# Kernel tuning notes

Hardware: AMD Instinct MI355X
Metric: run time of the kernel (lower is better)

The kernel has to match this reference:

```python
import jax, jax.numpy as jnp
import numpy as np

K, D, B, T = 512, 256, 32, 4096

def setup_inputs() -> dict:
    key = jax.random.key(0)
    k1, k2 = jax.random.split(key)
    z_e_x = jax.random.normal(k1, (B, D, T), dtype=jnp.float32)
    # nn.Embedding weight init uniform(-1/K, 1/K)
    emb_weight = jax.random.uniform(k2, (K, D), dtype=jnp.float32, minval=-1.0 / K, maxval=1.0 / K)
    return {"z_e_x": z_e_x, "emb_weight": emb_weight}

def reference(z_e_x, emb_weight):
    # forward(): permute [B,D,T] -> [B,T,D], nearest-codebook indices
    z = jnp.transpose(z_e_x, (0, 2, 1))  # [B, T, D]
    # squared L2 distances: ||z||^2 - 2 z.W^T + ||W||^2  -> [B, T, K]
    z_sq = jnp.sum(z * z, axis=-1, keepdims=True)           # [B, T, 1]
    w_sq = jnp.sum(emb_weight * emb_weight, axis=-1)        # [K]
    cross = jnp.einsum('btd,kd->btk', z, emb_weight)        # [B, T, K]
    dists = z_sq - 2.0 * cross + w_sq[None, None, :]
    latents = jnp.argmin(dists, axis=-1)                    # [B, T] int
    return latents
```

## Files before the change

kernel.cpp:

```cpp
#include <hip/hip_runtime.h>
#include <math.h>

#define NK 512
#define DD 256
#define NB 32
#define NT 4096

typedef __attribute__((ext_vector_type(8))) _Float16 f16x8;
typedef __attribute__((ext_vector_type(4))) float f32x4;

#define MARGIN 1.5e-4f
#define DCH 16
#define NCH 16
#define ASTR 536
#define PCAP   524288
#define PBCAP  2048

__device__ __forceinline__ unsigned short f16bits(float x) {
    _Float16 h = (_Float16)x;
    unsigned short s;
    __builtin_memcpy(&s, &h, 2);
    return s;
}

__global__ __launch_bounds__(512) void prep_kernel(const float* __restrict__ W,
                                                   unsigned short* __restrict__ Wpp,
                                                   float* __restrict__ wsq,
                                                   int* __restrict__ gcnt,
                                                   int* __restrict__ pcnt,
                                                   int* __restrict__ oflow) {
    const int bx = blockIdx.x;
    const int k  = threadIdx.x;
    if (bx < NCH) {
        const int d0 = bx * DCH;
        float w[16];
        const float4* src4 = (const float4*)(W + (size_t)k * DD + d0);
        #pragma unroll
        for (int q = 0; q < 4; ++q) {
            float4 v = src4[q];
            w[4 * q + 0] = v.x; w[4 * q + 1] = v.y; w[4 * q + 2] = v.z; w[4 * q + 3] = v.w;
        }
        __align__(16) unsigned int dw[16];
        #pragma unroll
        for (int j = 0; j < 16; ++j) {
            unsigned short s = f16bits(w[j] * 4096.0f);
            dw[j] = (unsigned int)s | ((unsigned int)s << 16);
        }
        unsigned short* dst = Wpp + ((size_t)bx * 512 + k) * 32;
        #pragma unroll
        for (int j = 0; j < 4; ++j) ((int4*)dst)[j] = ((const int4*)dw)[j];
    } else {
        const float4* row = (const float4*)(W + (size_t)k * DD);
        double s = 0.0;
        #pragma unroll 8
        for (int i = 0; i < DD / 4; ++i) {
            float4 v = row[i];
            s += (double)v.x * v.x + (double)v.y * v.y + (double)v.z * v.z + (double)v.w * v.w;
        }
        wsq[k] = (float)s;
        if (k == 0) *gcnt = 0;
        if (k == 1) *pcnt = 0;
        if (k == 2) *oflow = 0;
    }
}

__global__ __launch_bounds__(256, 2) void vq_phase1(const float* __restrict__ Z,
                                                    const unsigned short* __restrict__ Wpp,
                                                    const float* __restrict__ wsq,
                                                    int* __restrict__ out,
                                                    int* __restrict__ gties,
                                                    int* __restrict__ gcnt,
                                                    unsigned long long* __restrict__ slots,
                                                    int* __restrict__ gpairs,
                                                    int* __restrict__ pcnt,
                                                    int* __restrict__ oflow) {
    __shared__ __align__(16) short As[64 * ASTR];
    __shared__ int lcnt, gbase, pcl, pbase_sh;

    const int tid  = threadIdx.x;
    const int wave = tid >> 6;
    const int lane = tid & 63;
    const int lm   = lane & 15;
    const int lq   = lane >> 4;
    const int nw   = wave;

    const int bx = blockIdx.x;
    const int b  = bx >> 6;
    const int t0 = (bx & 63) * 64;

    const int t_l = tid & 63;
    const int dgs = tid >> 6;

    const float* zcol = Z + (size_t)b * DD * NT + t0 + t_l;

    if (tid == 0) { lcnt = 0; pcl = 0; }

    double zacc = 0.0;
    #pragma unroll
    for (int half = 0; half < 2; ++half) {
        float zv[32];
        #pragma unroll
        for (int j = 0; j < 32; ++j)
            zv[j] = zcol[(size_t)(dgs * 64 + half * 32 + j) * NT];
        #pragma unroll
        for (int j = 0; j < 32; ++j)
            zacc = fma((double)zv[j], (double)zv[j], zacc);
        #pragma unroll
        for (int j0 = 0; j0 < 32; j0 += 4) {
            __align__(16) unsigned int u[4];
            #pragma unroll
            for (int q = 0; q < 4; ++q) {
                float z = zv[j0 + q];
                _Float16 zh = (_Float16)z;
                float rz = z - (float)zh;
                unsigned short hs, ls;
                __builtin_memcpy(&hs, &zh, 2);
                ls = f16bits(rz);
                u[q] = (unsigned int)hs | ((unsigned int)ls << 16);
            }
            *(int4*)&As[t_l * ASTR + (dgs * 64 + half * 32 + j0) * 2] = *(const int4*)u;
        }
    }
    __syncthreads();

    const unsigned short* wb = Wpp + ((size_t)(nw * 128 + lm) * 32) + lq * 8;

    f32x4 acc[4][8];
    #pragma unroll
    for (int mt = 0; mt < 4; ++mt)
        #pragma unroll
        for (int nt = 0; nt < 8; ++nt)
            acc[mt][nt] = (f32x4){0.f, 0.f, 0.f, 0.f};

    int4 bv0[8], bv1[8];
    #pragma unroll
    for (int nt = 0; nt < 8; ++nt)
        bv0[nt] = *(const int4*)(wb + nt * 512);

    #pragma unroll
    for (int c = 0; c < NCH; ++c) {
        int4* cur = (c & 1) ? bv1 : bv0;
        int4* nxt = (c & 1) ? bv0 : bv1;
        if (c < NCH - 1) {
            const unsigned short* wp = wb + (size_t)(c + 1) * 16384;
            #pragma unroll
            for (int nt = 0; nt < 8; ++nt)
                nxt[nt] = *(const int4*)(wp + nt * 512);
        }
        f16x8 a[4];
        #pragma unroll
        for (int mt = 0; mt < 4; ++mt)
            a[mt] = *(const f16x8*)&As[(mt * 16 + lm) * ASTR + c * 32 + lq * 8];
        #pragma unroll
        for (int mt = 0; mt < 4; ++mt)
            #pragma unroll
            for (int nt = 0; nt < 8; ++nt)
                acc[mt][nt] = __builtin_amdgcn_mfma_f32_16x16x32_f16(
                    a[mt], *(const f16x8*)&cur[nt], acc[mt][nt], 0, 0, 0);
    }

    __syncthreads();
    char* base = (char*)As;
    double* zred  = (double*)base;
    float*  zf    = (float*)(base + 2048);
    float*  qf    = (float*)(base + 2304);
    int*    tia   = (int*)(base + 2560);
    int*    ltok  = (int*)(base + 2816);
    float*  cb1   = (float*)(base + 3072);
    float*  cb2   = (float*)(base + 4096);
    int*    cbi   = (int*)(base + 5120);
    int*    plist = (int*)(base + 6144);

    zred[dgs * 64 + t_l] = zacc;
    __syncthreads();
    if (tid < 64) {
        double s = zred[tid];
        #pragma unroll
        for (int p = 1; p < 4; ++p) s += zred[p * 64 + tid];
        zf[tid] = (float)s;
    }
    __syncthreads();

    float wq[8];
    #pragma unroll
    for (int nt = 0; nt < 8; ++nt)
        wq[nt] = wsq[nw * 128 + nt * 16 + lm];
    const int kbase = nw * 128 + lm;

    #pragma unroll
    for (int mt = 0; mt < 4; ++mt) {
        #pragma unroll
        for (int r = 0; r < 4; ++r) {
            float zz = zf[mt * 16 + lq * 4 + r];
            float q1 = INFINITY, q2 = INFINITY;
            int i1 = 0x7fffffff;
            #pragma unroll
            for (int nt = 0; nt < 8; ++nt) {
                float c2   = __fmul_rn(acc[mt][nt][r], 4.8828125e-4f);
                float dist = __fadd_rn(__fsub_rn(zz, c2), wq[nt]);
                int kk = kbase + nt * 16;
                if (dist < q1 || (dist == q1 && kk < i1)) { q2 = q1; q1 = dist; i1 = kk; }
                else if (dist < q2) q2 = dist;
            }
            #pragma unroll
            for (int mk = 1; mk <= 8; mk <<= 1) {
                float o1 = __shfl_xor(q1, mk);
                float o2 = __shfl_xor(q2, mk);
                int   oi = __shfl_xor(i1, mk);
                if (o1 < q1 || (o1 == q1 && oi < i1)) { q2 = fminf(q1, o2); q1 = o1; i1 = oi; }
                else { q2 = fminf(o1, q2); }
            }
            if (lm == 0) {
                int m = mt * 16 + lq * 4 + r;
                cb1[m * 4 + nw] = q1;
                cb2[m * 4 + nw] = q2;
                cbi[m * 4 + nw] = i1;
            }
        }
    }
    __syncthreads();
    if (tid < 64) {
        float q1 = cb1[tid * 4], q2 = cb2[tid * 4];
        int   i1 = cbi[tid * 4];
        #pragma unroll
        for (int p = 1; p < 4; ++p) {
            float c1 = cb1[tid * 4 + p], c2v = cb2[tid * 4 + p];
            int   ci = cbi[tid * 4 + p];
            if (c1 < q1 || (c1 == q1 && ci < i1)) { q2 = fminf(q1, c2v); q1 = c1; i1 = ci; }
            else { q2 = fminf(q2, c1); }
        }
        out[(size_t)b * NT + t0 + tid] = i1;
        qf[tid] = q1;
        int ta = -1;
        if (q2 - q1 <= MARGIN) {
            ta = atomicAdd(&lcnt, 1);
            ltok[ta] = tid;
        }
        tia[tid] = ta;
    }
    __syncthreads();
    const int nloc = lcnt;
    if (nloc == 0) return;

    if (tid == 0) gbase = atomicAdd(gcnt, nloc);
    __syncthreads();

    if (tid < nloc) {
        gties[gbase + tid] = b * NT + t0 + ltok[tid];
        slots[gbase + tid] = 0xFFFFFFFFFFFFFFFFULL;
    }

    #pragma unroll
    for (int mt = 0; mt < 4; ++mt) {
        #pragma unroll
        for (int r = 0; r < 4; ++r) {
            const int tok = mt * 16 + lq * 4 + r;
            const int ta  = tia[tok];
            if (ta < 0) continue;
            const int ti  = gbase + ta;
            const float thr = qf[tok] + MARGIN;
            const float zz  = zf[tok];
            #pragma unroll
            for (int nt = 0; nt < 8; ++nt) {
                float c2   = __fmul_rn(acc[mt][nt][r], 4.8828125e-4f);
                float dist = __fadd_rn(__fsub_rn(zz, c2), wq[nt]);
                if (dist <= thr) {
                    int p = atomicAdd(&pcl, 1);
                    if (p < PBCAP) plist[p] = (ti << 9) | (kbase + nt * 16);
                }
            }
        }
    }
    __syncthreads();
    if (tid == 0) {
        int take = pcl;
        int bs = atomicAdd(pcnt, take);
        pbase_sh = bs;
        if (take > PBCAP || bs + take > PCAP) *oflow = 1;
    }
    __syncthreads();
    {
        int take = pcl; if (take > PBCAP) take = PBCAP;
        for (int j = tid; j < take; j += 256) {
            int gp = pbase_sh + j;
            if (gp < PCAP) gpairs[gp] = plist[j];
        }
    }
}

__global__ __launch_bounds__(256) void vq_fix_pairs(const float* __restrict__ Z,
                                                    const float* __restrict__ W,
                                                    const float* __restrict__ wsq,
                                                    const int* __restrict__ gties,
                                                    const int* __restrict__ gpairs,
                                                    const int* __restrict__ pcnt,
                                                    unsigned long long* __restrict__ slots) {
    int np = *pcnt;
    if (np > PCAP) np = PCAP;
    for (int j = blockIdx.x * 256 + threadIdx.x; j < np; j += (int)gridDim.x * 256) {
        const int p  = gpairs[j];
        const int ti = p >> 9;
        const int k  = p & 511;
        const int bt = gties[ti];
        const int bb = bt >> 12, t = bt & 4095;
        const float* zc = Z + (size_t)bb * DD * NT + t;
        const float4* wr = (const float4*)(W + (size_t)k * DD);

        double tot = 0.0;
        float a8 = 0.f;
        for (int seg = 0; seg < 32; ++seg) {
            float zv[8];
            #pragma unroll
            for (int jj = 0; jj < 8; ++jj)
                zv[jj] = zc[(size_t)(seg * 8 + jj) * NT];
            float4 w4a = wr[seg * 2];
            float4 w4b = wr[seg * 2 + 1];
            double s = 0.0;
            #pragma unroll
            for (int jj = 0; jj < 8; ++jj) {
                double zz = (double)zv[jj];
                s = fma(zz, zz, s);
            }
            tot += s;
            a8 = fmaf(zv[0], w4a.x, a8);
            a8 = fmaf(zv[1], w4a.y, a8);
            a8 = fmaf(zv[2], w4a.z, a8);
            a8 = fmaf(zv[3], w4a.w, a8);
            a8 = fmaf(zv[4], w4b.x, a8);
            a8 = fmaf(zv[5], w4b.y, a8);
            a8 = fmaf(zv[6], w4b.z, a8);
            a8 = fmaf(zv[7], w4b.w, a8);
        }
        float zqv = (float)tot;
        float da = __fadd_rn(__fsub_rn(zqv, __fmul_rn(2.0f, a8)), wsq[k]);
        unsigned long long key =
            ((unsigned long long)__float_as_uint(da) << 32) | (unsigned int)k;
        atomicMin(&slots[ti], key);
    }
}

__global__ __launch_bounds__(256) void vq_final(const int* __restrict__ gties,
                                                const int* __restrict__ gcnt,
                                                const int* __restrict__ oflow,
                                                const unsigned long long* __restrict__ slots,
                                                int* __restrict__ out) {
    if (*oflow) return;
    const int n = *gcnt;
    for (int j = blockIdx.x * 256 + threadIdx.x; j < n; j += (int)gridDim.x * 256) {
        out[gties[j]] = (int)(slots[j] & 511ULL);
    }
}

__global__ __launch_bounds__(256) void vq_fix(const float* __restrict__ Z,
                                              const float* __restrict__ W,
                                              const float* __restrict__ wsq,
                                              const int* __restrict__ gties,
                                              const int* __restrict__ gcnt,
                                              int* __restrict__ out,
                                              const int* __restrict__ oflow) {
    if (oflow != nullptr && *oflow == 0) return;

    __shared__ __align__(16) float Zs[8][256];
    __shared__ double pz[8][32];
    __shared__ float  zsqs[8];
    __shared__ int    bts[8];
    __shared__ float  rv[8][4];
    __shared__ int    ri[8][4];

    const int tid  = threadIdx.x;
    const int lane = tid & 63;
    const int wvx  = tid >> 6;
    const int n    = *gcnt;

    for (int base = blockIdx.x * 8; base < n; base += (int)gridDim.x * 8) {
        const int m = (n - base < 8) ? (n - base) : 8;
        __syncthreads();
        if (tid < 8) bts[tid] = gties[base + ((tid < m) ? tid : 0)];
        __syncthreads();

        #pragma unroll
        for (int i = 0; i < 8; ++i) {
            if (i < m) {
                int tb = bts[i];
                int bb = tb >> 12, t = tb & 4095;
                Zs[i][tid] = Z[(size_t)bb * DD * NT + (size_t)tid * NT + t];
            }
        }
        __syncthreads();

        {
            int i = tid >> 5, seg = tid & 31;
            double s = 0.0;
            #pragma unroll
            for (int j = 0; j < 8; ++j) {
                double zz = (double)Zs[i][seg * 8 + j];
                s = fma(zz, zz, s);
            }
            pz[i][seg] = s;
        }
        __syncthreads();
        if (tid < 8) {
            double s = 0.0;
            #pragma unroll
            for (int j = 0; j < 32; ++j) s += pz[tid][j];
            zsqs[tid] = (float)s;
        }
        __syncthreads();

        float da[2][8];
        #pragma unroll
        for (int rr = 0; rr < 2; ++rr) {
            int k = tid + rr * 256;
            const float4* wr = (const float4*)(W + (size_t)k * DD);
            float a8[8];
            #pragma unroll
            for (int i = 0; i < 8; ++i) a8[i] = 0.f;
            #pragma unroll 2
            for (int q = 0; q < 64; ++q) {
                float4 w4 = wr[q];
                #pragma unroll
                for (int i = 0; i < 8; ++i) {
                    float4 z4 = *(const float4*)&Zs[i][4 * q];
                    a8[i] = fmaf(z4.x, w4.x, a8[i]);
                    a8[i] = fmaf(z4.y, w4.y, a8[i]);
                    a8[i] = fmaf(z4.z, w4.z, a8[i]);
                    a8[i] = fmaf(z4.w, w4.w, a8[i]);
                }
            }
            float wqv = wsq[k];
            #pragma unroll
            for (int i = 0; i < 8; ++i)
                da[rr][i] = __fadd_rn(__fsub_rn(zsqs[i], __fmul_rn(2.0f, a8[i])), wqv);
        }

        #pragma unroll
        for (int i = 0; i < 8; ++i) {
            float v = da[0][i]; int ix = tid;
            if (da[1][i] < v) { v = da[1][i]; ix = tid + 256; }
            #pragma unroll
            for (int mk = 1; mk <= 32; mk <<= 1) {
                float ov = __shfl_xor(v, mk);
                int   oi = __shfl_xor(ix, mk);
                if (ov < v || (ov == v && oi < ix)) { v = ov; ix = oi; }
            }
            if (lane == 0) { rv[i][wvx] = v; ri[i][wvx] = ix; }
        }
        __syncthreads();
        if (tid < 8 && tid < m) {
            float v = INFINITY; int ix = 0x7fffffff;
            #pragma unroll
            for (int w = 0; w < 4; ++w) {
                if (rv[tid][w] < v || (rv[tid][w] == v && ri[tid][w] < ix)) {
                    v = rv[tid][w]; ix = ri[tid][w];
                }
            }
            out[bts[tid]] = ix;
        }
    }
}

__global__ __launch_bounds__(256, 2) void vq_phase1_reg(const float* __restrict__ Z,
                                                        const unsigned short* __restrict__ Wpp,
                                                        const float* __restrict__ wsq,
                                                        int* __restrict__ out,
                                                        int* __restrict__ gties,
                                                        int* __restrict__ gcnt) {
    __shared__ __align__(16) short As[64 * ASTR];
    __shared__ int lcnt, gbase;

    const int tid  = threadIdx.x;
    const int wave = tid >> 6;
    const int lane = tid & 63;
    const int lm   = lane & 15;
    const int lq   = lane >> 4;
    const int nw   = wave;

    const int bx = blockIdx.x;
    const int b  = bx >> 6;
    const int t0 = (bx & 63) * 64;

    const int t_l = tid & 63;
    const int dgs = tid >> 6;

    const float* zcol = Z + (size_t)b * DD * NT + t0 + t_l;

    if (tid == 0) lcnt = 0;

    double zacc = 0.0;
    #pragma unroll
    for (int half = 0; half < 2; ++half) {
        float zv[32];
        #pragma unroll
        for (int j = 0; j < 32; ++j)
            zv[j] = zcol[(size_t)(dgs * 64 + half * 32 + j) * NT];
        #pragma unroll
        for (int j = 0; j < 32; ++j)
            zacc = fma((double)zv[j], (double)zv[j], zacc);
        #pragma unroll
        for (int j0 = 0; j0 < 32; j0 += 4) {
            __align__(16) unsigned int u[4];
            #pragma unroll
            for (int q = 0; q < 4; ++q) {
                float z = zv[j0 + q];
                _Float16 zh = (_Float16)z;
                float rz = z - (float)zh;
                unsigned short hs, ls;
                __builtin_memcpy(&hs, &zh, 2);
                ls = f16bits(rz);
                u[q] = (unsigned int)hs | ((unsigned int)ls << 16);
            }
            *(int4*)&As[t_l * ASTR + (dgs * 64 + half * 32 + j0) * 2] = *(const int4*)u;
        }
    }
    __syncthreads();

    const unsigned short* wb = Wpp + ((size_t)(nw * 128 + lm) * 32) + lq * 8;

    f32x4 acc[4][8];
    #pragma unroll
    for (int mt = 0; mt < 4; ++mt)
        #pragma unroll
        for (int nt = 0; nt < 8; ++nt)
            acc[mt][nt] = (f32x4){0.f, 0.f, 0.f, 0.f};

    int4 bv0[8], bv1[8];
    #pragma unroll
    for (int nt = 0; nt < 8; ++nt)
        bv0[nt] = *(const int4*)(wb + nt * 512);

    #pragma unroll
    for (int c = 0; c < NCH; ++c) {
        int4* cur = (c & 1) ? bv1 : bv0;
        int4* nxt = (c & 1) ? bv0 : bv1;
        if (c < NCH - 1) {
            const unsigned short* wp = wb + (size_t)(c + 1) * 16384;
            #pragma unroll
            for (int nt = 0; nt < 8; ++nt)
                nxt[nt] = *(const int4*)(wp + nt * 512);
        }
        f16x8 a[4];
        #pragma unroll
        for (int mt = 0; mt < 4; ++mt)
            a[mt] = *(const f16x8*)&As[(mt * 16 + lm) * ASTR + c * 32 + lq * 8];
        #pragma unroll
        for (int mt = 0; mt < 4; ++mt)
            #pragma unroll
            for (int nt = 0; nt < 8; ++nt)
                acc[mt][nt] = __builtin_amdgcn_mfma_f32_16x16x32_f16(
                    a[mt], *(const f16x8*)&cur[nt], acc[mt][nt], 0, 0, 0);
    }

    __syncthreads();
    double* zred = (double*)As;
    float*  zf   = (float*)(As + 1024);
    float*  cb1  = (float*)(As + 1536);
    float*  cb2  = (float*)(As + 2048);
    int*    cbi  = (int*)(As + 2560);
    int*    llist = (int*)(As + 3072);

    zred[dgs * 64 + t_l] = zacc;
    __syncthreads();
    if (tid < 64) {
        double s = zred[tid];
        #pragma unroll
        for (int p = 1; p < 4; ++p) s += zred[p * 64 + tid];
        zf[tid] = (float)s;
    }
    __syncthreads();

    float wq[8];
    #pragma unroll
    for (int nt = 0; nt < 8; ++nt)
        wq[nt] = wsq[nw * 128 + nt * 16 + lm];
    const int kbase = nw * 128 + lm;

    #pragma unroll
    for (int mt = 0; mt < 4; ++mt) {
        #pragma unroll
        for (int r = 0; r < 4; ++r) {
            float zz = zf[mt * 16 + lq * 4 + r];
            float q1 = INFINITY, q2 = INFINITY;
            int i1 = 0x7fffffff;
            #pragma unroll
            for (int nt = 0; nt < 8; ++nt) {
                float c2   = __fmul_rn(acc[mt][nt][r], 4.8828125e-4f);
                float dist = __fadd_rn(__fsub_rn(zz, c2), wq[nt]);
                int kk = kbase + nt * 16;
                if (dist < q1 || (dist == q1 && kk < i1)) { q2 = q1; q1 = dist; i1 = kk; }
                else if (dist < q2) q2 = dist;
            }
            #pragma unroll
            for (int mk = 1; mk <= 8; mk <<= 1) {
                float o1 = __shfl_xor(q1, mk);
                float o2 = __shfl_xor(q2, mk);
                int   oi = __shfl_xor(i1, mk);
                if (o1 < q1 || (o1 == q1 && oi < i1)) { q2 = fminf(q1, o2); q1 = o1; i1 = oi; }
                else { q2 = fminf(o1, q2); }
            }
            if (lm == 0) {
                int m = mt * 16 + lq * 4 + r;
                cb1[m * 4 + nw] = q1;
                cb2[m * 4 + nw] = q2;
                cbi[m * 4 + nw] = i1;
            }
        }
    }
    __syncthreads();
    if (tid < 64) {
        float q1 = cb1[tid * 4], q2 = cb2[tid * 4];
        int   i1 = cbi[tid * 4];
        #pragma unroll
        for (int p = 1; p < 4; ++p) {
            float c1 = cb1[tid * 4 + p], c2v = cb2[tid * 4 + p];
            int   ci = cbi[tid * 4 + p];
            if (c1 < q1 || (c1 == q1 && ci < i1)) { q2 = fminf(q1, c2v); q1 = c1; i1 = ci; }
            else { q2 = fminf(q2, c1); }
        }
        out[(size_t)b * NT + t0 + tid] = i1;
        if (q2 - q1 <= MARGIN) {
            int p = atomicAdd(&lcnt, 1);
            llist[p] = b * NT + t0 + tid;
        }
    }
    __syncthreads();
    if (tid == 0) gbase = (lcnt > 0) ? atomicAdd(gcnt, lcnt) : 0;
    __syncthreads();
    if (tid < lcnt) gties[gbase + tid] = llist[tid];
}

#define BT 128
#define BK 128
#define DCHUNK 32
#define NKC (NK / BK)
#define NDC (DD / DCHUNK)
#define WSTR (BK + 4)

__global__ __launch_bounds__(256) void vq_fallback(const float* __restrict__ Z,
                                                   const float* __restrict__ W,
                                                   int* __restrict__ out) {
    __shared__ __align__(16) float Zs[DCHUNK * BT];
    __shared__ __align__(16) float Ws[DCHUNK * WSTR];
    __shared__ float wsqs[NK];

    const int tid = threadIdx.x;
    const int tx  = tid & 15;
    const int ty  = tid >> 4;
    const int b   = blockIdx.y;
    const int t0  = blockIdx.x * BT;

    for (int k = tid; k < NK; k += 256) {
        const float4* row = (const float4*)(W + (size_t)k * DD);
        double s = 0.0;
        for (int i = 0; i < DD / 4; ++i) {
            float4 v = row[i];
            s += (double)v.x * v.x + (double)v.y * v.y + (double)v.z * v.z + (double)v.w * v.w;
        }
        wsqs[k] = (float)s;
    }

    const float* Zb = Z + (size_t)b * DD * NT + t0;

    float best[8]; int bidx[8];
    #pragma unroll
    for (int a = 0; a < 8; ++a) { best[a] = INFINITY; bidx[a] = 0x7fffffff; }
    double zsqd[8];
    #pragma unroll
    for (int a = 0; a < 8; ++a) zsqd[a] = 0.0;
    float zsqf[8];

    for (int kc = 0; kc < NKC; ++kc) {
        float acc[8][8];
        #pragma unroll
        for (int a = 0; a < 8; ++a)
            #pragma unroll
            for (int c = 0; c < 8; ++c) acc[a][c] = 0.f;

        for (int dc = 0; dc < NDC; ++dc) {
            const int d0 = dc * DCHUNK;
            __syncthreads();
            #pragma unroll
            for (int i = 0; i < 4; ++i) {
                int f  = tid + i * 256;
                int r  = f >> 5;
                int c4 = f & 31;
                float4 v = *(const float4*)(Zb + (size_t)(d0 + r) * NT + c4 * 4);
                *(float4*)(&Zs[r * BT + c4 * 4]) = v;
            }
            #pragma unroll
            for (int i = 0; i < 4; ++i) {
                int u  = tid + i * 256;
                int k  = u >> 3;
                int rg = u & 7;
                float4 v = *(const float4*)(W + (size_t)(kc * BK + k) * DD + d0 + rg * 4);
                Ws[(rg * 4 + 0) * WSTR + k] = v.x;
                Ws[(rg * 4 + 1) * WSTR + k] = v.y;
                Ws[(rg * 4 + 2) * WSTR + k] = v.z;
                Ws[(rg * 4 + 3) * WSTR + k] = v.w;
            }
            __syncthreads();
            #pragma unroll 4
            for (int d = 0; d < DCHUNK; ++d) {
                float4 z0 = *(const float4*)(&Zs[d * BT + ty * 8]);
                float4 z1 = *(const float4*)(&Zs[d * BT + ty * 8 + 4]);
                float4 w0 = *(const float4*)(&Ws[d * WSTR + tx * 8]);
                float4 w1 = *(const float4*)(&Ws[d * WSTR + tx * 8 + 4]);
                float za[8] = {z0.x, z0.y, z0.z, z0.w, z1.x, z1.y, z1.z, z1.w};
                float wa[8] = {w0.x, w0.y, w0.z, w0.w, w1.x, w1.y, w1.z, w1.w};
                if (kc == 0) {
                    #pragma unroll
                    for (int a = 0; a < 8; ++a)
                        zsqd[a] = fma((double)za[a], (double)za[a], zsqd[a]);
                }
                #pragma unroll
                for (int a = 0; a < 8; ++a)
                    #pragma unroll
                    for (int c = 0; c < 8; ++c)
                        acc[a][c] = fmaf(za[a], wa[c], acc[a][c]);
            }
        }
        if (kc == 0) {
            #pragma unroll
            for (int a = 0; a < 8; ++a) zsqf[a] = (float)zsqd[a];
        }
        #pragma unroll
        for (int c = 0; c < 8; ++c) {
            int   kg = kc * BK + tx * 8 + c;
            float wqv = wsqs[kg];
            #pragma unroll
            for (int a = 0; a < 8; ++a) {
                float c2   = __fmul_rn(2.0f, acc[a][c]);
                float s    = __fsub_rn(zsqf[a], c2);
                float dist = __fadd_rn(s, wqv);
                if (dist < best[a] || (dist == best[a] && kg < bidx[a])) {
                    best[a] = dist; bidx[a] = kg;
                }
            }
        }
    }
    __syncthreads();
    float* redv = Zs;
    int*   redi = (int*)Ws;
    #pragma unroll
    for (int a = 0; a < 8; ++a) {
        int tl2 = ty * 8 + a;
        redv[tl2 * 16 + tx] = best[a];
        redi[tl2 * 16 + tx] = bidx[a];
    }
    __syncthreads();
    if (tid < BT) {
        float bv = INFINITY; int bi = 0x7fffffff;
        #pragma unroll
        for (int j = 0; j < 16; ++j) {
            float v = redv[tid * 16 + j];
            int   i = redi[tid * 16 + j];
            if (v < bv || (v == bv && i < bi)) { bv = v; bi = i; }
        }
        out[(size_t)b * NT + t0 + tid] = bi;
    }
}

extern "C" void kernel_launch(void* const* d_in, const int* in_sizes, int n_in,
                              void* d_out, int out_size, void* d_ws, size_t ws_size,
                              hipStream_t stream) {
    const float* Z = (const float*)d_in[0];
    const float* W = (const float*)d_in[1];
    int* out = (int*)d_out;

    const size_t OFF_WSQ  = 0;
    const size_t OFF_CNT  = 2048;
    const size_t OFF_PCNT = 2052;
    const size_t OFF_OFL  = 2056;
    const size_t OFF_WPP  = 4096;
    const size_t OFF_TIE  = OFF_WPP + 524288;
    const size_t OFF_SLOT = OFF_TIE + 524288;
    const size_t OFF_PAIR = OFF_SLOT + 1048576;
    const size_t NEED_BIG = OFF_PAIR + (size_t)PCAP * 4;

    const size_t T2_WSQ = 0;
    const size_t T2_CNT = 2048;
    const size_t T2_WPP = 4096;
    const size_t T2_TIE = T2_WPP + 524288;
    const size_t NEED_T2 = T2_TIE + 524288;

    if (ws_size >= NEED_BIG) {
        float* wsq  = (float*)((char*)d_ws + OFF_WSQ);
        int*   gcnt = (int*)((char*)d_ws + OFF_CNT);
        int*   pcnt = (int*)((char*)d_ws + OFF_PCNT);
        int*   ofl  = (int*)((char*)d_ws + OFF_OFL);
        unsigned short* wpp = (unsigned short*)((char*)d_ws + OFF_WPP);
        int*   gties = (int*)((char*)d_ws + OFF_TIE);
        unsigned long long* slots = (unsigned long long*)((char*)d_ws + OFF_SLOT);
        int*   gpairs = (int*)((char*)d_ws + OFF_PAIR);

        prep_kernel<<<dim3(NCH + 1), dim3(512), 0, stream>>>(W, wpp, wsq, gcnt, pcnt, ofl);
        vq_phase1<<<dim3(2048), dim3(256), 0, stream>>>(Z, wpp, wsq, out, gties, gcnt,
                                                        slots, gpairs, pcnt, ofl);
        vq_fix_pairs<<<dim3(256), dim3(256), 0, stream>>>(Z, W, wsq, gties, gpairs, pcnt, slots);
        vq_fix<<<dim3(256), dim3(256), 0, stream>>>(Z, W, wsq, gties, gcnt, out, ofl);
        vq_final<<<dim3(256), dim3(256), 0, stream>>>(gties, gcnt, ofl, slots, out);
    } else if (ws_size >= NEED_T2) {
        float* wsq  = (float*)((char*)d_ws + T2_WSQ);
        int*   gcnt = (int*)((char*)d_ws + T2_CNT);
        unsigned short* wpp = (unsigned short*)((char*)d_ws + T2_WPP);
        int*   gties = (int*)((char*)d_ws + T2_TIE);

        prep_kernel<<<dim3(NCH + 1), dim3(512), 0, stream>>>(W, wpp, wsq, gcnt, gcnt, gcnt);
        vq_phase1_reg<<<dim3(2048), dim3(256), 0, stream>>>(Z, wpp, wsq, out, gties, gcnt);
        vq_fix<<<dim3(256), dim3(256), 0, stream>>>(Z, W, wsq, gties, gcnt, out, nullptr);
    } else {
        vq_fallback<<<dim3(NT / BT, NB), dim3(256), 0, stream>>>(Z, W, out);
    }
}
```

Baseline: 359.8 us.

## Stage tied-token Z columns contiguously in phase1 for faster pair refinement

Phase1 now gathers the full 256-dim Z column for each near-tie token into shared memory, writes it as a contiguous row to a workspace buffer, and precomputes its squared norm in double. The pair-fix kernel then reads contiguous float4 rows and reuses the stored norm instead of doing strided column gathers and recomputing the norm for every candidate pair. The fix grid is doubled. This adds gather and write work in phase1 for blocks that have ties, and blocks exceeding the new capacity limits set the overflow flag and fall back to the slower fix path.

Measured after the change: 358.9 us. No clear change (-0.3%).

```diff
diff --git a/kernel.cpp b/kernel.cpp
--- a/kernel.cpp
+++ b/kernel.cpp
@@ -15,6 +15,8 @@
 #define ASTR 536
 #define PCAP   524288
 #define PBCAP  2048
+#define ZCROWS 65536
+#define ZCMAX  48
 
 __device__ __forceinline__ unsigned short f16bits(float x) {
     _Float16 h = (_Float16)x;
@@ -70,6 +72,8 @@
                                                     int* __restrict__ out,
                                                     int* __restrict__ gties,
                                                     int* __restrict__ gcnt,
+                                                    float* __restrict__ Zc,
+                                                    float* __restrict__ zq,
                                                     unsigned long long* __restrict__ slots,
                                                     int* __restrict__ gpairs,
                                                     int* __restrict__ pcnt,
@@ -170,6 +174,7 @@
     float*  cb2   = (float*)(base + 4096);
     int*    cbi   = (int*)(base + 5120);
     int*    plist = (int*)(base + 6144);
+    float*  colbuf = (float*)(base + 14336);
 
     zred[dgs * 64 + t_l] = zacc;
     __syncthreads();
@@ -245,10 +250,14 @@
     if (tid == 0) gbase = atomicAdd(gcnt, nloc);
     __syncthreads();
 
-    if (tid < nloc) {
-        gties[gbase + tid] = b * NT + t0 + ltok[tid];
-        slots[gbase + tid] = 0xFFFFFFFFFFFFFFFFULL;
-    }
+    if (tid < nloc) gties[gbase + tid] = b * NT + t0 + ltok[tid];
+
+    const bool okzc = (gbase + nloc <= ZCROWS) && (nloc <= ZCMAX);
+    if (!okzc) {
+        if (tid == 0) *oflow = 1;
+        return;
+    }
+    if (tid < nloc) slots[gbase + tid] = 0xFFFFFFFFFFFFFFFFULL;
 
     #pragma unroll
     for (int mt = 0; mt < 4; ++mt) {
@@ -286,12 +295,40 @@
             if (gp < PCAP) gpairs[gp] = plist[j];
         }
     }
+
+    {
+        const int i  = tid & 63;
+        const int dw = tid >> 6;
+        for (int du = 0; du < 64; ++du) {
+            const int d = du * 4 + dw;
+            if (i < nloc)
+                colbuf[i * 257 + d] =
+                    Z[(size_t)b * DD * NT + (size_t)d * NT + (t0 + ltok[i])];
+        }
+    }
+    __syncthreads();
+    for (int i = 0; i < nloc; ++i)
+        Zc[(size_t)(gbase + i) * 256 + tid] = colbuf[i * 257 + tid];
+    if (tid < nloc) {
+        const float* cp = colbuf + tid * 257;
+        double tot = 0.0;
+        for (int seg = 0; seg < 32; ++seg) {
+            double s = 0.0;
+            #pragma unroll
+            for (int jj = 0; jj < 8; ++jj) {
+                double zz = (double)cp[seg * 8 + jj];
+                s = fma(zz, zz, s);
+            }
+            tot += s;
+        }
+        zq[gbase + tid] = (float)tot;
+    }
 }
 
-__global__ __launch_bounds__(256) void vq_fix_pairs(const float* __restrict__ Z,
-                                                    const float* __restrict__ W,
+__global__ __launch_bounds__(256) void vq_fix_pairs(const float* __restrict__ W,
                                                     const float* __restrict__ wsq,
-                                                    const int* __restrict__ gties,
+                                                    const float* __restrict__ Zc,
+                                                    const float* __restrict__ zq,
                                                     const int* __restrict__ gpairs,
                                                     const int* __restrict__ pcnt,
                                                     unsigned long long* __restrict__ slots) {
@@ -301,38 +338,20 @@
         const int p  = gpairs[j];
         const int ti = p >> 9;
         const int k  = p & 511;
-        const int bt = gties[ti];
-        const int bb = bt >> 12, t = bt & 4095;
-        const float* zc = Z + (size_t)bb * DD * NT + t;
+        if (ti >= ZCROWS) continue;
+        const float4* zr = (const float4*)(Zc + (size_t)ti * 256);
         const float4* wr = (const float4*)(W + (size_t)k * DD);
-
-        double tot = 0.0;
         float a8 = 0.f;
-        for (int seg = 0; seg < 32; ++seg) {
-            float zv[8];
-            #pragma unroll
-            for (int jj = 0; jj < 8; ++jj)
-                zv[jj] = zc[(size_t)(seg * 8 + jj) * NT];
-            float4 w4a = wr[seg * 2];
-            float4 w4b = wr[seg * 2 + 1];
-            double s = 0.0;
-            #pragma unroll
-            for (int jj = 0; jj < 8; ++jj) {
-                double zz = (double)zv[jj];
-                s = fma(zz, zz, s);
-            }
-            tot += s;
-            a8 = fmaf(zv[0], w4a.x, a8);
-            a8 = fmaf(zv[1], w4a.y, a8);
-            a8 = fmaf(zv[2], w4a.z, a8);
-            a8 = fmaf(zv[3], w4a.w, a8);
-            a8 = fmaf(zv[4], w4b.x, a8);
-            a8 = fmaf(zv[5], w4b.y, a8);
-            a8 = fmaf(zv[6], w4b.z, a8);
-            a8 = fmaf(zv[7], w4b.w, a8);
-        }
-        float zqv = (float)tot;
-        float da = __fadd_rn(__fsub_rn(zqv, __fmul_rn(2.0f, a8)), wsq[k]);
+        #pragma unroll 4
+        for (int q = 0; q < 64; ++q) {
+            float4 w4 = wr[q];
+            float4 z4 = zr[q];
+            a8 = fmaf(z4.x, w4.x, a8);
+            a8 = fmaf(z4.y, w4.y, a8);
+            a8 = fmaf(z4.z, w4.z, a8);
+            a8 = fmaf(z4.w, w4.w, a8);
+        }
+        float da = __fadd_rn(__fsub_rn(zq[ti], __fmul_rn(2.0f, a8)), wsq[k]);
         unsigned long long key =
             ((unsigned long long)__float_as_uint(da) << 32) | (unsigned int)k;
         atomicMin(&slots[ti], key);
@@ -770,11 +789,13 @@
     const size_t OFF_CNT  = 2048;
     const size_t OFF_PCNT = 2052;
     const size_t OFF_OFL  = 2056;
-    const size_t OFF_WPP  = 4096;
+    const size_t OFF_ZQ   = 4096;
+    const size_t OFF_WPP  = OFF_ZQ + 524288;
     const size_t OFF_TIE  = OFF_WPP + 524288;
     const size_t OFF_SLOT = OFF_TIE + 524288;
     const size_t OFF_PAIR = OFF_SLOT + 1048576;
-    const size_t NEED_BIG = OFF_PAIR + (size_t)PCAP * 4;
+    const size_t OFF_ZC   = OFF_PAIR + (size_t)PCAP * 4;
+    const size_t NEED_BIG = OFF_ZC + (size_t)ZCROWS * 1024;
 
     const size_t T2_WSQ = 0;
     const size_t T2_CNT = 2048;
@@ -787,15 +808,17 @@
         int*   gcnt = (int*)((char*)d_ws + OFF_CNT);
         int*   pcnt = (int*)((char*)d_ws + OFF_PCNT);
         int*   ofl  = (int*)((char*)d_ws + OFF_OFL);
+        float* zq   = (float*)((char*)d_ws + OFF_ZQ);
         unsigned short* wpp = (unsigned short*)((char*)d_ws + OFF_WPP);
         int*   gties = (int*)((char*)d_ws + OFF_TIE);
         unsigned long long* slots = (unsigned long long*)((char*)d_ws + OFF_SLOT);
         int*   gpairs = (int*)((char*)d_ws + OFF_PAIR);
+        float* zc   = (float*)((char*)d_ws + OFF_ZC);
 
         prep_kernel<<<dim3(NCH + 1), dim3(512), 0, stream>>>(W, wpp, wsq, gcnt, pcnt, ofl);
         vq_phase1<<<dim3(2048), dim3(256), 0, stream>>>(Z, wpp, wsq, out, gties, gcnt,
-                                                        slots, gpairs, pcnt, ofl);
-        vq_fix_pairs<<<dim3(256), dim3(256), 0, stream>>>(Z, W, wsq, gties, gpairs, pcnt, slots);
+                                                        zc, zq, slots, gpairs, pcnt, ofl);
+        vq_fix_pairs<<<dim3(512), dim3(256), 0, stream>>>(W, wsq, zc, zq, gpairs, pcnt, slots);
         vq_fix<<<dim3(256), dim3(256), 0, stream>>>(Z, W, wsq, gties, gcnt, out, ofl);
         vq_final<<<dim3(256), dim3(256), 0, stream>>>(gties, gcnt, ofl, slots, out);
     } else if (ws_size >= NEED_T2) {
```
